# Kernel optimization log

Measured on AMD Instinct MI355X. Metric: run time of the kernel, lower is better.

## Reference

```python
import jax, jax.numpy as jnp
import numpy as np

EPS = 1e-6
NEG_SLOPE = 0.01  # torch LeakyReLU default

def ln(x, g, b):
    m = jnp.mean(x, axis=-1, keepdims=True)
    v = jnp.mean((x - m) ** 2, axis=-1, keepdims=True)
    return (x - m) / jnp.sqrt(v + EPS) * g + b

def leaky(x):
    return jnp.where(x >= 0, x, NEG_SLOPE * x)

def setup_inputs() -> dict:
    B, L, F, H, NH, LBL = 8, 1024, 1024, 256, 8, 4766
    key = jax.random.key(0)
    ks = jax.random.split(key, 16)
    def lin(k, i, o, s=0.03):
        kw, kb = jax.random.split(k)
        return jax.random.normal(kw, (i, o), jnp.float32) * s, jnp.zeros((o,), jnp.float32)
    w_in, b_in = lin(ks[0], F, H)
    w_h, b_h = lin(ks[1], H, H)
    a_w1, a_b1 = lin(ks[2], H, 64)
    a_w2, a_b2 = lin(ks[3], 64, NH)
    o_w1, o_b1 = lin(ks[4], NH * H, NH * H)
    o_w2, o_b2 = lin(ks[5], NH * H, LBL)
    CM = (jax.random.uniform(ks[6], (LBL, LBL)) < 0.002).astype(jnp.float32)
    CM = jnp.maximum(CM, jnp.eye(LBL, dtype=jnp.float32))
    return {
        'h_V': jax.random.normal(ks[7], (B, L, F), jnp.float32),
        'mask': jnp.ones((B, L), jnp.int32),
        'ln0_g': jnp.ones((F,), jnp.float32), 'ln0_b': jnp.zeros((F,), jnp.float32),
        'w_in': w_in, 'b_in': b_in,
        'ln1_g': jnp.ones((H,), jnp.float32), 'ln1_b': jnp.zeros((H,), jnp.float32),
        'w_h': w_h, 'b_h': b_h,
        'ln2_g': jnp.ones((H,), jnp.float32), 'ln2_b': jnp.zeros((H,), jnp.float32),
        'a_w1': a_w1, 'a_b1': a_b1,
        'a_lng': jnp.ones((64,), jnp.float32), 'a_lnb': jnp.zeros((64,), jnp.float32),
        'a_w2': a_w2, 'a_b2': a_b2,
        'o_w1': o_w1, 'o_b1': o_b1,
        'o_lng': jnp.ones((NH * H,), jnp.float32), 'o_lnb': jnp.zeros((NH * H,), jnp.float32),
        'o_w2': o_w2, 'o_b2': o_b2,
        'CM': CM,
    }

def reference(h_V, mask, ln0_g, ln0_b, w_in, b_in, ln1_g, ln1_b, w_h, b_h,
              ln2_g, ln2_b, a_w1, a_b1, a_lng, a_lnb, a_w2, a_b2,
              o_w1, o_b1, o_lng, o_lnb, o_w2, o_b2, CM):
    B = h_V.shape[0]
    # input + hidden blocks (eval mode: dropout is identity)
    x = ln(h_V, ln0_g, ln0_b)
    x = leaky(x @ w_in + b_in)
    x = ln(x, ln1_g, ln1_b)
    x = leaky(x @ w_h + b_h)
    x = ln(x, ln2_g, ln2_b)                      # [B,L,H]
    # multi-head attention pooling over sequence
    a = leaky(x @ a_w1 + a_b1)
    a = ln(a, a_lng, a_lnb)
    a = a @ a_w2 + a_b2                          # [B,L,NH]
    a = jnp.where(mask[:, :, None] == 0, jnp.float32(-1e9), a)
    a = jax.nn.softmax(a, axis=1)
    h = jnp.einsum('blh,bld->bhd', a, x).reshape(B, -1)  # [B,NH*H]
    # output block
    h = leaky(h @ o_w1 + o_b1)
    h = ln(h, o_lng, o_lnb)
    p = jax.nn.sigmoid(h @ o_w2 + o_b2)          # [B,LBL]
    # GO-hierarchy max-product propagation (eval path)
    out = jnp.max(p[:, None, :] * CM[None, :, :], axis=-1)  # [B,LBL]
    return out.astype(jnp.float32)
```

## Files before the change

kernel.cpp:

```cpp
#include <hip/hip_runtime.h>
#include <hip/hip_bf16.h>
#include <cstdint>

#define B_   8
#define L_   1024
#define F_   1024
#define H_   256
#define NH_  8
#define LBL_ 4766
#define M_   (B_*L_)
#define OD_  (NH_*H_)
#define NCM  (LBL_*LBL_)
#define MP_EPB 16384
#define MP_NB  ((NCM + MP_EPB - 1) / MP_EPB)
#define NCH  32

typedef unsigned short u16;
typedef unsigned int   u32;
typedef __attribute__((ext_vector_type(8))) short short8;
typedef __attribute__((ext_vector_type(4))) float float4v;

#define BF16_ONES_PAIR 0x3f803f80u

__device__ __forceinline__ float bf2f(u32 u) { return __uint_as_float(u << 16); }
__device__ __forceinline__ u16 f2bf(float f) {
    u32 u = __float_as_uint(f);
    u32 r = 0x7fffu + ((u >> 16) & 1u);
    return (u16)((u + r) >> 16);
}

struct f8 { float v[8]; };

__device__ __forceinline__ float ldS(const void* p, size_t i, bool bf) {
    return bf ? bf2f(((const u16*)p)[i]) : ((const float*)p)[i];
}
__device__ __forceinline__ float4 ld4(const void* p, size_t i, bool bf) {
    if (bf) {
        uint2 u = *(const uint2*)((const u16*)p + i);
        return make_float4(bf2f(u.x & 0xffff), bf2f(u.x >> 16),
                           bf2f(u.y & 0xffff), bf2f(u.y >> 16));
    }
    return *(const float4*)((const float*)p + i);
}
__device__ __forceinline__ f8 ld8(const void* p, size_t i, bool bf) {
    f8 r;
    if (bf) {
        uint4 u = *(const uint4*)((const u16*)p + i);
        r.v[0]=bf2f(u.x&0xffff); r.v[1]=bf2f(u.x>>16);
        r.v[2]=bf2f(u.y&0xffff); r.v[3]=bf2f(u.y>>16);
        r.v[4]=bf2f(u.z&0xffff); r.v[5]=bf2f(u.z>>16);
        r.v[6]=bf2f(u.w&0xffff); r.v[7]=bf2f(u.w>>16);
    } else {
        const float* q = (const float*)p + i;
        float4 a = *(const float4*)q, b = *(const float4*)(q+4);
        r.v[0]=a.x; r.v[1]=a.y; r.v[2]=a.z; r.v[3]=a.w;
        r.v[4]=b.x; r.v[5]=b.y; r.v[6]=b.z; r.v[7]=b.w;
    }
    return r;
}

__device__ __forceinline__ float wave_sum(float v) {
    #pragma unroll
    for (int m = 1; m < 64; m <<= 1) v += __shfl_xor(v, m, 64);
    return v;
}
__device__ __forceinline__ float wave_max(float v) {
    #pragma unroll
    for (int m = 1; m < 64; m <<= 1) v = fmaxf(v, __shfl_xor(v, m, 64));
    return v;
}
__device__ __forceinline__ float blk_sum(float v, float* sh) {
    v = wave_sum(v);
    int w = threadIdx.x >> 6, nw = blockDim.x >> 6;
    if ((threadIdx.x & 63) == 0) sh[w] = v;
    __syncthreads();
    float s = sh[0];
    for (int i = 1; i < nw; ++i) s += sh[i];
    __syncthreads();
    return s;
}
__device__ __forceinline__ float blk_max(float v, float* sh) {
    v = wave_max(v);
    int w = threadIdx.x >> 6, nw = blockDim.x >> 6;
    if ((threadIdx.x & 63) == 0) sh[w] = v;
    __syncthreads();
    float s = sh[0];
    for (int i = 1; i < nw; ++i) s = fmaxf(s, sh[i]);
    __syncthreads();
    return s;
}

__global__ __launch_bounds__(256) void prep_k(const void* __restrict__ hv,
        const void* __restrict__ g0, const void* __restrict__ b0, u16* __restrict__ x0,
        const void* __restrict__ w_in, u16* __restrict__ wt1,
        const void* __restrict__ w_h,  u16* __restrict__ wt2,
        const void* __restrict__ aw1,  u16* __restrict__ wt3,
        float* __restrict__ zA,
        const u32* __restrict__ probe) {
    __shared__ u16 tile[64][65];
    bool bf = (probe[0] == BF16_ONES_PAIR);
    int blk = blockIdx.x, t = threadIdx.x;
    if (blk < M_/4) {
        int row = (blk << 2) + (t >> 6);
        int l = t & 63;
        size_t base = (size_t)row * F_;
        float4 vv[4];
        float s = 0.f, q = 0.f;
        #pragma unroll
        for (int j = 0; j < 4; ++j) {
            float4 v = ld4(hv, base + l * 4 + j * 256, bf);
            vv[j] = v;
            s += v.x + v.y + v.z + v.w;
            q += v.x*v.x + v.y*v.y + v.z*v.z + v.w*v.w;
        }
        s = wave_sum(s);
        q = wave_sum(q);
        float mean = s * (1.f / F_);
        float rstd = rsqrtf(q * (1.f / F_) - mean * mean + 1e-6f);
        #pragma unroll
        for (int j = 0; j < 4; ++j) {
            int off = l * 4 + j * 256;
            float4 gg = ld4(g0, off, bf);
            float4 bb = ld4(b0, off, bf);
            float4 v = vv[j];
            u32 o0 = f2bf((v.x - mean) * rstd * gg.x + bb.x)
                   | ((u32)f2bf((v.y - mean) * rstd * gg.y + bb.y) << 16);
            u32 o1 = f2bf((v.z - mean) * rstd * gg.z + bb.z)
                   | ((u32)f2bf((v.w - mean) * rstd * gg.w + bb.w) << 16);
            *(uint2*)(x0 + base + off) = make_uint2(o0, o1);
        }
        return;
    }
    blk -= M_/4;
    const void* W = nullptr; u16* WT = nullptr; int K = 0, N = 0, kt = 0, nt = 0;
    if (blk < 64)      { W = w_in; WT = wt1; K = F_; N = H_; kt = blk & 15; nt = blk >> 4; }
    else if (blk < 80) { int j = blk - 64; W = w_h; WT = wt2; K = H_; N = H_; kt = j & 3; nt = j >> 2; }
    else if (blk < 84) { int j = blk - 80; W = aw1; WT = wt3; K = H_; N = 64; kt = j; nt = 0; }
    else {
        int j = blk - 84;
        float4* p = (float4*)zA;
        for (int i = j * 256 + t; i < 8192; i += 4096) p[i] = make_float4(0,0,0,0);
        return;
    }
    int kt0 = kt * 64, nt0 = nt * 64;
    int r = t >> 2, cq = (t & 3) * 16;
    #pragma unroll
    for (int j = 0; j < 4; ++j) {
        float4 v = ld4(W, (size_t)(kt0 + r) * N + nt0 + cq + j * 4, bf);
        tile[r][cq + j*4 + 0] = f2bf(v.x);
        tile[r][cq + j*4 + 1] = f2bf(v.y);
        tile[r][cq + j*4 + 2] = f2bf(v.z);
        tile[r][cq + j*4 + 3] = f2bf(v.w);
    }
    __syncthreads();
    #pragma unroll
    for (int j = 0; j < 4; ++j) {
        int k = cq + j * 4;
        u32 a0 = tile[k+0][r], a1 = tile[k+1][r], a2 = tile[k+2][r], a3 = tile[k+3][r];
        uint2 o; o.x = a0 | (a1 << 16); o.y = a2 | (a3 << 16);
        *(uint2*)(WT + (size_t)(nt0 + r) * K + kt0 + k) = o;
    }
}

__global__ __launch_bounds__(256) void gemm_mfma(const u16* __restrict__ Ap, int amode,
        const float2* __restrict__ statin, const void* __restrict__ g,
        const void* __restrict__ bta, const u16* __restrict__ WT,
        const void* __restrict__ bias, u16* __restrict__ C,
        float* __restrict__ statout, int M, int N, int K,
        const u32* __restrict__ probe) {
    __shared__ short8 As[2][64][5];
    __shared__ short8 Bs[2][64][5];
    bool pbf = (probe[0] == BF16_ONES_PAIR);
    int t = threadIdx.x;
    int m0 = blockIdx.x * 64, n0 = blockIdx.y * 64;
    int r = t >> 2, kq = t & 3;
    int l = t & 63, w = t >> 6;
    int q = l >> 4, ml = l & 15;
    float4v acc[4];
    #pragma unroll
    for (int nt = 0; nt < 4; ++nt)
        #pragma unroll
        for (int i = 0; i < 4; ++i) acc[nt][i] = 0.f;
    float stm = 0.f, str = 1.f;
    if (amode == 1) {
        float2 st = statin[m0 + r];
        float mm = st.x * (1.f / K);
        stm = mm;
        str = rsqrtf(st.y * (1.f / K) - mm * mm + 1e-6f);
    }
    const size_t arow = (size_t)(m0 + r) * K;
    const size_t brow = (size_t)(n0 + r) * K;
    auto loadA = [&](int kk) -> short8 {
        if (amode == 1) {
            f8 a  = ld8(Ap, arow + kk, true);
            f8 gg = ld8(g, kk, pbf);
            f8 bb = ld8(bta, kk, pbf);
            short8 pa;
            #pragma unroll
            for (int j = 0; j < 8; ++j)
                pa[j] = (short)f2bf((a.v[j] - stm) * str * gg.v[j] + bb.v[j]);
            return pa;
        }
        return *(const short8*)(Ap + arow + kk);
    };
    {
        short8 pa = loadA(kq * 8);
        short8 pb = *(const short8*)(WT + brow + kq * 8);
        As[0][r][kq] = pa;
        Bs[0][r][kq] = pb;
    }
    __syncthreads();
    int nIt = K >> 5, cur = 0;
    for (int it = 0; it < nIt; ++it) {
        bool more = (it + 1 < nIt);
        short8 na, nb;
        if (more) {
            int kk = (it + 1) * 32 + kq * 8;
            na = loadA(kk);
            nb = *(const short8*)(WT + brow + kk);
        }
        short8 af = As[cur][w * 16 + ml][q];
        #pragma unroll
        for (int nt = 0; nt < 4; ++nt)
            acc[nt] = __builtin_amdgcn_mfma_f32_16x16x32_bf16(af, Bs[cur][nt*16 + ml][q],
                                                              acc[nt], 0, 0, 0);
        if (more) {
            As[cur ^ 1][r][kq] = na;
            Bs[cur ^ 1][r][kq] = nb;
            __syncthreads();
            cur ^= 1;
        }
    }
    float ov[4][4];
    #pragma unroll
    for (int nt = 0; nt < 4; ++nt) {
        int nn = n0 + nt * 16 + ml;
        float bv = ldS(bias, nn, pbf);
        #pragma unroll
        for (int reg = 0; reg < 4; ++reg) {
            float v = acc[nt][reg] + bv;
            v = v >= 0.f ? v : 0.01f * v;
            ov[nt][reg] = v;
            C[(size_t)(m0 + w * 16 + q * 4 + reg) * N + nn] = f2bf(v);
        }
    }
    if (statout) {
        #pragma unroll
        for (int reg = 0; reg < 4; ++reg) {
            float sv = ov[0][reg] + ov[1][reg] + ov[2][reg] + ov[3][reg];
            float qv = ov[0][reg]*ov[0][reg] + ov[1][reg]*ov[1][reg]
                     + ov[2][reg]*ov[2][reg] + ov[3][reg]*ov[3][reg];
            #pragma unroll
            for (int mk = 1; mk < 16; mk <<= 1) {
                sv += __shfl_xor(sv, mk, 64);
                qv += __shfl_xor(qv, mk, 64);
            }
            if (ml == 0) {
                int row = m0 + w * 16 + q * 4 + reg;
                atomicAdd(&statout[2 * row],     sv);
                atomicAdd(&statout[2 * row + 1], qv);
            }
        }
    }
}

__global__ __launch_bounds__(256) void gemm3_attn_k(const u16* __restrict__ Ap,
        const float2* __restrict__ statin, const void* __restrict__ g,
        const void* __restrict__ bta, const u16* __restrict__ WT,
        const void* __restrict__ bias,
        const void* __restrict__ alng, const void* __restrict__ alnb,
        const void* __restrict__ aw2, const void* __restrict__ ab2,
        const int* __restrict__ mask, float* __restrict__ lg,
        const u32* __restrict__ probe) {
    __shared__ short8 As[2][64][5];
    __shared__ short8 Bs[2][64][5];
    __shared__ float at[64][65];
    __shared__ float w2s[512];
    __shared__ float b2s[8];
    __shared__ float gs[64], bs[64];
    bool pbf = (probe[0] == BF16_ONES_PAIR);
    const int K = 256;
    int t = threadIdx.x;
    int m0 = blockIdx.x * 64;
    int r = t >> 2, kq = t & 3;
    int l = t & 63, w = t >> 6;
    int q = l >> 4, ml = l & 15;
    float4v acc[4];
    #pragma unroll
    for (int nt = 0; nt < 4; ++nt)
        #pragma unroll
        for (int i = 0; i < 4; ++i) acc[nt][i] = 0.f;
    float2 st = statin[m0 + r];
    float stm = st.x * (1.f / K);
    float str = rsqrtf(st.y * (1.f / K) - stm * stm + 1e-6f);
    const size_t arow = (size_t)(m0 + r) * K;
    const size_t brow = (size_t)r * K;
    auto loadA = [&](int kk) -> short8 {
        f8 a  = ld8(Ap, arow + kk, true);
        f8 gg = ld8(g, kk, pbf);
        f8 bb = ld8(bta, kk, pbf);
        short8 pa;
        #pragma unroll
        for (int j = 0; j < 8; ++j)
            pa[j] = (short)f2bf((a.v[j] - stm) * str * gg.v[j] + bb.v[j]);
        return pa;
    };
    {
        short8 pa = loadA(kq * 8);
        short8 pb = *(const short8*)(WT + brow + kq * 8);
        As[0][r][kq] = pa;
        Bs[0][r][kq] = pb;
    }
    __syncthreads();
    int cur = 0;
    #pragma unroll
    for (int it = 0; it < 8; ++it) {
        bool more = (it < 7);
        short8 na, nb;
        if (more) {
            int kk = (it + 1) * 32 + kq * 8;
            na = loadA(kk);
            nb = *(const short8*)(WT + brow + kk);
        }
        short8 af = As[cur][w * 16 + ml][q];
        #pragma unroll
        for (int nt = 0; nt < 4; ++nt)
            acc[nt] = __builtin_amdgcn_mfma_f32_16x16x32_bf16(af, Bs[cur][nt*16 + ml][q],
                                                              acc[nt], 0, 0, 0);
        if (more) {
            As[cur ^ 1][r][kq] = na;
            Bs[cur ^ 1][r][kq] = nb;
            __syncthreads();
            cur ^= 1;
        }
    }
    for (int i = t; i < 512; i += 256) w2s[i] = ldS(aw2, i, pbf);
    if (t < 8) b2s[t] = ldS(ab2, t, pbf);
    if (t < 64) { gs[t] = ldS(alng, t, pbf); bs[t] = ldS(alnb, t, pbf); }
    #pragma unroll
    for (int nt = 0; nt < 4; ++nt) {
        int nn = nt * 16 + ml;
        float bv = ldS(bias, nn, pbf);
        #pragma unroll
        for (int reg = 0; reg < 4; ++reg) {
            float v = acc[nt][reg] + bv;
            v = v >= 0.f ? v : 0.01f * v;
            at[w * 16 + q * 4 + reg][nn] = v;
        }
    }
    __syncthreads();
    int row = t >> 2, s4 = t & 3;
    float av[16];
    float sum = 0.f, sq = 0.f;
    #pragma unroll
    for (int j = 0; j < 16; ++j) {
        float v = at[row][s4 * 16 + j];
        av[j] = v; sum += v; sq += v * v;
    }
    sum += __shfl_xor(sum, 1, 64); sum += __shfl_xor(sum, 2, 64);
    sq  += __shfl_xor(sq, 1, 64);  sq  += __shfl_xor(sq, 2, 64);
    float mr = sum * (1.f / 64);
    float rr = rsqrtf(sq * (1.f / 64) - mr * mr + 1e-6f);
    float val[16];
    #pragma unroll
    for (int j = 0; j < 16; ++j)
        val[j] = (av[j] - mr) * rr * gs[s4 * 16 + j] + bs[s4 * 16 + j];
    float hv[8];
    #pragma unroll
    for (int h = 0; h < 8; ++h) {
        float p = 0.f;
        #pragma unroll
        for (int j = 0; j < 16; ++j) p += val[j] * w2s[(s4 * 16 + j) * 8 + h];
        p += __shfl_xor(p, 1, 64);
        p += __shfl_xor(p, 2, 64);
        hv[h] = p + b2s[h];
    }
    if (s4 == 0) {
        int gr = m0 + row;
        bool mz = (mask[gr] == 0);
        int bb_ = gr >> 10, ll = gr & 1023;
        #pragma unroll
        for (int h = 0; h < 8; ++h) {
            float v = mz ? -1e9f : hv[h];
            lg[((size_t)bb_ * NH_ + h) * L_ + ll] = v;
        }
    }
}

__global__ __launch_bounds__(1024) void attnpool_k(const float* __restrict__ lg,
        const float2* __restrict__ st2, const u16* __restrict__ x2,
        const void* __restrict__ g, const void* __restrict__ b,
        float* __restrict__ hp, const u32* __restrict__ probe) {
    __shared__ float aw_s[1024];
    __shared__ float part[16][256];
    __shared__ float sh[16];
    bool pbf = (probe[0] == BF16_ONES_PAIR);
    int bh = blockIdx.x, t = threadIdx.x;
    int bb = bh >> 3;
    float v = lg[(size_t)bh * L_ + t];
    float mx = blk_max(v, sh);
    float e = expf(v - mx);
    float s = blk_sum(e, sh);
    float inv = 1.f / s;
    float2 st = st2[(bb << 10) + t];
    float m = st.x * (1.f / 256);
    float r = rsqrtf(st.y * (1.f / 256) - m * m + 1e-6f);
    float aw = e * inv * r;
    aw_s[t] = aw;
    float c1 = blk_sum(aw * m, sh);
    int chunk = t >> 6, d0 = (t & 63) * 4;
    const u16* xb = x2 + ((size_t)(bb << 10) + chunk * 64) * 256;
    const float* awc = aw_s + chunk * 64;
    float a0 = 0.f, a1 = 0.f, a2 = 0.f, a3 = 0.f;
    #pragma unroll 8
    for (int i = 0; i < 64; ++i) {
        uint2 u = *(const uint2*)(xb + (size_t)i * 256 + d0);
        float wv = awc[i];
        a0 += wv * bf2f(u.x & 0xffff);
        a1 += wv * bf2f(u.x >> 16);
        a2 += wv * bf2f(u.y & 0xffff);
        a3 += wv * bf2f(u.y >> 16);
    }
    *(float4*)&part[chunk][d0] = make_float4(a0, a1, a2, a3);
    __syncthreads();
    if (t < 256) {
        float S = 0.f;
        #pragma unroll
        for (int c = 0; c < 16; ++c) S += part[c][t];
        hp[(size_t)bh * 256 + t] = (S - c1) * ldS(g, t, pbf) + ldS(b, t, pbf);
    }
}

template<int KC>
__global__ __launch_bounds__(256) void gemv_ilp_part_k(const float* __restrict__ hv,
        const void* __restrict__ W, float* __restrict__ part, int K, int N,
        const u32* __restrict__ probe) {
    __shared__ float hs[8 * KC];
    bool bf = (probe[0] == BF16_ONES_PAIR);
    int t = threadIdx.x;
    int kb = blockIdx.y * KC;
    for (int i = t; i < 8 * KC; i += 256) {
        int r = i / KC, k = i & (KC - 1);
        hs[i] = hv[(size_t)r * K + kb + k];
    }
    __syncthreads();
    int c0 = (blockIdx.x * 256 + t) * 2;
    if (c0 >= N) return;
    float a[8][2] = {};
    if (bf) {
        const u16* Wp = (const u16*)W;
        #pragma unroll
        for (int h = 0; h < KC / 32; ++h) {
            u32 wr[32];
            #pragma unroll
            for (int i = 0; i < 32; ++i)
                wr[i] = *(const u32*)(Wp + (size_t)(kb + h * 32 + i) * N + c0);
            #pragma unroll
            for (int i = 0; i < 32; ++i) {
                float w0 = bf2f(wr[i] & 0xffff), w1 = bf2f(wr[i] >> 16);
                #pragma unroll
                for (int r = 0; r < 8; ++r) {
                    float hh = hs[r * KC + h * 32 + i];
                    a[r][0] += hh * w0; a[r][1] += hh * w1;
                }
            }
        }
    } else {
        const float* Wp = (const float*)W;
        #pragma unroll
        for (int h = 0; h < KC / 16; ++h) {
            float2 wr[16];
            #pragma unroll
            for (int i = 0; i < 16; ++i)
                wr[i] = *(const float2*)(Wp + (size_t)(kb + h * 16 + i) * N + c0);
            #pragma unroll
            for (int i = 0; i < 16; ++i) {
                #pragma unroll
                for (int r = 0; r < 8; ++r) {
                    float hh = hs[r * KC + h * 16 + i];
                    a[r][0] += hh * wr[i].x; a[r][1] += hh * wr[i].y;
                }
            }
        }
    }
    float* dst = part + ((size_t)blockIdx.y * 8) * N + c0;
    bool ok1 = (c0 + 1 < N);
    #pragma unroll
    for (int r = 0; r < 8; ++r) {
        if (ok1) *(float2*)(dst + (size_t)r * N) = make_float2(a[r][0], a[r][1]);
        else dst[(size_t)r * N] = a[r][0];
    }
}

__global__ __launch_bounds__(1024) void out_ln_k(const float* __restrict__ part,
        float* __restrict__ h, const void* __restrict__ bias,
        const void* __restrict__ g, const void* __restrict__ b,
        const u32* __restrict__ probe) {
    __shared__ float sh[16];
    bool bf = (probe[0] == BF16_ONES_PAIR);
    int row = blockIdx.x, t = threadIdx.x;
    float v[2];
    float s = 0.f, q = 0.f;
    #pragma unroll
    for (int i = 0; i < 2; ++i) {
        int c = t + i * 1024;
        float pv[NCH];
        #pragma unroll
        for (int ch = 0; ch < NCH; ++ch)
            pv[ch] = part[((size_t)ch * 8 + row) * OD_ + c];
        #pragma unroll
        for (int st = NCH / 2; st >= 1; st >>= 1)
            #pragma unroll
            for (int j = 0; j < NCH; ++j)
                if (j < st) pv[j] += pv[j + st];
        float x = ldS(bias, c, bf) + pv[0];
        x = x >= 0.f ? x : 0.01f * x;
        v[i] = x; s += x; q += x * x;
    }
    s = blk_sum(s, sh) * (1.f / OD_);
    q = blk_sum(q, sh) * (1.f / OD_);
    float rstd = rsqrtf(q - s * s + 1e-6f);
    #pragma unroll
    for (int i = 0; i < 2; ++i) {
        int c = t + i * 1024;
        h[(size_t)row * OD_ + c] = (v[i] - s) * rstd * ldS(g, c, bf) + ldS(b, c, bf);
    }
}

__global__ __launch_bounds__(256) void sigmoid_t_k(const float* __restrict__ part,
        const void* __restrict__ bias, float* __restrict__ pt,
        float* __restrict__ out, const u32* __restrict__ probe) {
    bool bf = (probe[0] == BF16_ONES_PAIR);
    int c = blockIdx.x * 256 + threadIdx.x;
    int r = blockIdx.y;
    if (c >= LBL_) return;
    float pv[NCH];
    #pragma unroll
    for (int ch = 0; ch < NCH; ++ch)
        pv[ch] = part[((size_t)ch * 8 + r) * LBL_ + c];
    #pragma unroll
    for (int st = NCH / 2; st >= 1; st >>= 1)
        #pragma unroll
        for (int j = 0; j < NCH; ++j)
            if (j < st) pv[j] += pv[j + st];
    float v = ldS(bias, c, bf) + pv[0];
    pt[(size_t)c * 8 + r] = 1.f / (1.f + expf(-v));
    out[(size_t)r * LBL_ + c] = 0.f;
}

__device__ __forceinline__ void mp_hit(u32 idx, float cmv,
        const float* __restrict__ pt, int* smax, u32 rowBase) {
    u32 i = idx / LBL_;
    u32 j = idx - i * LBL_;
    const float4* pj = (const float4*)(pt + (size_t)j * 8);
    float4 pa = pj[0], pb = pj[1];
    int base = (int)(i - rowBase) * 8;
    atomicMax(&smax[base + 0], __float_as_int(pa.x * cmv));
    atomicMax(&smax[base + 1], __float_as_int(pa.y * cmv));
    atomicMax(&smax[base + 2], __float_as_int(pa.z * cmv));
    atomicMax(&smax[base + 3], __float_as_int(pa.w * cmv));
    atomicMax(&smax[base + 4], __float_as_int(pb.x * cmv));
    atomicMax(&smax[base + 5], __float_as_int(pb.y * cmv));
    atomicMax(&smax[base + 6], __float_as_int(pb.z * cmv));
    atomicMax(&smax[base + 7], __float_as_int(pb.w * cmv));
}

__global__ __launch_bounds__(256) void maxprod3_k(const float* __restrict__ pt,
        const void* __restrict__ CM, float* __restrict__ out,
        const u32* __restrict__ probe) {
    __shared__ int smax[6 * 8];
    bool bf = (probe[0] == BF16_ONES_PAIR);
    int t = threadIdx.x;
    size_t blockStart = (size_t)blockIdx.x * MP_EPB;
    u32 rowBase = (u32)(blockStart / LBL_);
    for (int i = t; i < 48; i += 256) smax[i] = 0;
    __syncthreads();
    if (bf) {
        const u16* cm = (const u16*)CM;
        uint4 ch[8];
        size_t i0[8];
        #pragma unroll
        for (int u = 0; u < 8; ++u) {
            size_t idx0 = blockStart + ((size_t)u * 256 + t) * 8;
            i0[u] = idx0;
            ch[u] = (idx0 + 8 <= NCM) ? *(const uint4*)(cm + idx0)
                                      : make_uint4(0, 0, 0, 0);
        }
        #pragma unroll
        for (int u = 0; u < 8; ++u) {
            size_t idx0 = i0[u];
            if (idx0 + 8 <= NCM) {
                uint4 c4 = ch[u];
                if ((c4.x | c4.y | c4.z | c4.w) == 0) continue;
                u32 hw[4] = {c4.x, c4.y, c4.z, c4.w};
                #pragma unroll
                for (int d = 0; d < 4; ++d) {
                    u32 lo = hw[d] & 0xffff, hi = hw[d] >> 16;
                    if (lo) mp_hit((u32)idx0 + d*2,     bf2f(lo), pt, smax, rowBase);
                    if (hi) mp_hit((u32)idx0 + d*2 + 1, bf2f(hi), pt, smax, rowBase);
                }
            } else if (idx0 < NCM) {
                for (u32 e = 0; e < (u32)(NCM - idx0); ++e) {
                    u16 h = cm[idx0 + e];
                    if (h) mp_hit((u32)idx0 + e, bf2f(h), pt, smax, rowBase);
                }
            }
        }
    } else {
        const float* cm = (const float*)CM;
        #pragma unroll
        for (int u = 0; u < 16; ++u) {
            size_t idx0 = blockStart + ((size_t)u * 256 + t) * 4;
            if (idx0 >= NCM) continue;
            float v[4];
            if (idx0 + 4 <= NCM) {
                float4 f = *(const float4*)(cm + idx0);
                v[0] = f.x; v[1] = f.y; v[2] = f.z; v[3] = f.w;
            } else {
                v[0] = v[1] = v[2] = v[3] = 0.f;
                for (u32 e = 0; e < (u32)(NCM - idx0); ++e) v[e] = cm[idx0 + e];
            }
            if (v[0] == 0.f && v[1] == 0.f && v[2] == 0.f && v[3] == 0.f) continue;
            #pragma unroll
            for (int e = 0; e < 4; ++e)
                if (v[e] != 0.f) mp_hit((u32)idx0 + e, v[e], pt, smax, rowBase);
        }
    }
    __syncthreads();
    size_t lastIdx = blockStart + MP_EPB - 1;
    if (lastIdx >= NCM) lastIdx = NCM - 1;
    int nrows = (int)((u32)(lastIdx / LBL_) - rowBase) + 1;
    for (int s = t; s < nrows * 8; s += 256) {
        int v = smax[s];
        if (v != 0) {
            int rr = s >> 3, b = s & 7;
            atomicMax((int*)(out + (size_t)b * LBL_ + rowBase + rr), v);
        }
    }
}

extern "C" void kernel_launch(void* const* d_in, const int* in_sizes, int n_in,
                              void* d_out, int out_size, void* d_ws, size_t ws_size,
                              hipStream_t stream) {
    const void* hv   = d_in[0];
    const int* mask  = (const int*)d_in[1];
    const void* ln0g = d_in[2];
    const void* ln0b = d_in[3];
    const void* w_in = d_in[4];
    const void* b_in = d_in[5];
    const void* ln1g = d_in[6];
    const void* ln1b = d_in[7];
    const void* w_h  = d_in[8];
    const void* b_h  = d_in[9];
    const void* ln2g = d_in[10];
    const void* ln2b = d_in[11];
    const void* aw1  = d_in[12];
    const void* ab1  = d_in[13];
    const void* alng = d_in[14];
    const void* alnb = d_in[15];
    const void* aw2  = d_in[16];
    const void* ab2  = d_in[17];
    const void* ow1  = d_in[18];
    const void* ob1  = d_in[19];
    const void* olng = d_in[20];
    const void* olnb = d_in[21];
    const void* ow2  = d_in[22];
    const void* ob2  = d_in[23];
    const void* CM   = d_in[24];
    const u32* probe = (const u32*)ln0g;
    float* out = (float*)d_out;

    float* f = (float*)d_ws;
    float2* st1 = (float2*)f;
    float2* st2 = st1 + 8192;
    float* lg    = f + 32768;
    float* hp    = lg + 65536;
    float* ha    = hp + 16384;
    float* part1 = ha + 16384;
    float* part2 = part1 + 524288;
    float* pt    = part2 + 1220096;
    u16* x0  = (u16*)(pt + 38128);
    u16* x1  = x0 + 8388608;
    u16* x2  = x1 + 2097152;
    u16* wt1 = x2 + 2097152;
    u16* wt2 = wt1 + 262144;
    u16* wt3 = wt2 + 65536;

    prep_k<<<M_/4 + 84 + 16, 256, 0, stream>>>(hv, ln0g, ln0b, x0,
                                               w_in, wt1, w_h, wt2, aw1, wt3,
                                               f, probe);
    gemm_mfma<<<dim3(M_/64, 4), 256, 0, stream>>>(x0, 2, nullptr, nullptr, nullptr,
                                                  wt1, b_in, x1, (float*)st1,
                                                  M_, H_, F_, probe);
    gemm_mfma<<<dim3(M_/64, 4), 256, 0, stream>>>(x1, 1, st1, ln1g, ln1b,
                                                  wt2, b_h, x2, (float*)st2,
                                                  M_, H_, H_, probe);
    gemm3_attn_k<<<M_/64, 256, 0, stream>>>(x2, st2, ln2g, ln2b, wt3, ab1,
                                            alng, alnb, aw2, ab2, mask, lg, probe);
    attnpool_k<<<B_*NH_, 1024, 0, stream>>>(lg, st2, x2, ln2g, ln2b, hp, probe);
    gemv_ilp_part_k<64><<<dim3(OD_/512, NCH), 256, 0, stream>>>(hp, ow1, part1,
                                                                OD_, OD_, probe);
    out_ln_k<<<B_, 1024, 0, stream>>>(part1, ha, ob1, olng, olnb, probe);
    gemv_ilp_part_k<64><<<dim3((LBL_+511)/512, NCH), 256, 0, stream>>>(ha, ow2, part2,
                                                                       OD_, LBL_, probe);
    sigmoid_t_k<<<dim3((LBL_+255)/256, 8), 256, 0, stream>>>(part2, ob2, pt, out, probe);
    maxprod3_k<<<MP_NB, 256, 0, stream>>>(pt, CM, out, probe);
}
```

Before: 332.6 us.

## Widen GEMM N-tile to 128 and replace stat atomics with per-tile partial writes

The gemm_mfma tile grows from 64x64 to 64x128, so each block does 8 MFMA accumulators per k-step and the A tile is loaded and LayerNorm-normalized half as often. Row-stat accumulation switches from atomicAdd into a zeroed buffer to plain stores of per-column-tile partials, which consumers (next GEMM, gemm3_attn, attnpool) sum from two slices. This removes the zero-init blocks in prep_k. The cost is halving the grid of the first two GEMMs to 256 blocks, which lowers occupancy on a 256-CU part, and adding accumulator registers.

```diff
diff --git a/kernel.cpp b/kernel.cpp
--- a/kernel.cpp
+++ b/kernel.cpp
@@ -95,7 +95,6 @@
         const void* __restrict__ w_in, u16* __restrict__ wt1,
         const void* __restrict__ w_h,  u16* __restrict__ wt2,
         const void* __restrict__ aw1,  u16* __restrict__ wt3,
-        float* __restrict__ zA,
         const u32* __restrict__ probe) {
     __shared__ u16 tile[64][65];
     bool bf = (probe[0] == BF16_ONES_PAIR);
@@ -135,13 +134,7 @@
     const void* W = nullptr; u16* WT = nullptr; int K = 0, N = 0, kt = 0, nt = 0;
     if (blk < 64)      { W = w_in; WT = wt1; K = F_; N = H_; kt = blk & 15; nt = blk >> 4; }
     else if (blk < 80) { int j = blk - 64; W = w_h; WT = wt2; K = H_; N = H_; kt = j & 3; nt = j >> 2; }
-    else if (blk < 84) { int j = blk - 80; W = aw1; WT = wt3; K = H_; N = 64; kt = j; nt = 0; }
-    else {
-        int j = blk - 84;
-        float4* p = (float4*)zA;
-        for (int i = j * 256 + t; i < 8192; i += 4096) p[i] = make_float4(0,0,0,0);
-        return;
-    }
+    else               { int j = blk - 80; W = aw1; WT = wt3; K = H_; N = 64; kt = j; nt = 0; }
     int kt0 = kt * 64, nt0 = nt * 64;
     int r = t >> 2, cq = (t & 3) * 16;
     #pragma unroll
@@ -169,27 +162,30 @@
         float* __restrict__ statout, int M, int N, int K,
         const u32* __restrict__ probe) {
     __shared__ short8 As[2][64][5];
-    __shared__ short8 Bs[2][64][5];
+    __shared__ short8 Bs[2][128][5];
     bool pbf = (probe[0] == BF16_ONES_PAIR);
     int t = threadIdx.x;
-    int m0 = blockIdx.x * 64, n0 = blockIdx.y * 64;
+    int m0 = blockIdx.x * 64, n0 = blockIdx.y * 128;
     int r = t >> 2, kq = t & 3;
+    int rb = t & 127, hb = t >> 7;
     int l = t & 63, w = t >> 6;
     int q = l >> 4, ml = l & 15;
-    float4v acc[4];
-    #pragma unroll
-    for (int nt = 0; nt < 4; ++nt)
+    float4v acc[8];
+    #pragma unroll
+    for (int nt = 0; nt < 8; ++nt)
         #pragma unroll
         for (int i = 0; i < 4; ++i) acc[nt][i] = 0.f;
     float stm = 0.f, str = 1.f;
     if (amode == 1) {
-        float2 st = statin[m0 + r];
-        float mm = st.x * (1.f / K);
+        float2 s0 = statin[m0 + r];
+        float2 s1 = statin[M + m0 + r];
+        float ssum = s0.x + s1.x, ssq = s0.y + s1.y;
+        float mm = ssum * (1.f / K);
         stm = mm;
-        str = rsqrtf(st.y * (1.f / K) - mm * mm + 1e-6f);
+        str = rsqrtf(ssq * (1.f / K) - mm * mm + 1e-6f);
     }
     const size_t arow = (size_t)(m0 + r) * K;
-    const size_t brow = (size_t)(n0 + r) * K;
+    const size_t brow = (size_t)(n0 + rb) * K + hb * 16;
     auto loadA = [&](int kk) -> short8 {
         if (amode == 1) {
             f8 a  = ld8(Ap, arow + kk, true);
@@ -205,35 +201,39 @@
     };
     {
         short8 pa = loadA(kq * 8);
-        short8 pb = *(const short8*)(WT + brow + kq * 8);
+        short8 pb0 = *(const short8*)(WT + brow);
+        short8 pb1 = *(const short8*)(WT + brow + 8);
         As[0][r][kq] = pa;
-        Bs[0][r][kq] = pb;
+        Bs[0][rb][2*hb]   = pb0;
+        Bs[0][rb][2*hb+1] = pb1;
     }
     __syncthreads();
     int nIt = K >> 5, cur = 0;
     for (int it = 0; it < nIt; ++it) {
         bool more = (it + 1 < nIt);
-        short8 na, nb;
+        short8 na, nb0, nb1;
         if (more) {
-            int kk = (it + 1) * 32 + kq * 8;
-            na = loadA(kk);
-            nb = *(const short8*)(WT + brow + kk);
+            int kk = (it + 1) * 32;
+            na  = loadA(kk + kq * 8);
+            nb0 = *(const short8*)(WT + brow + kk);
+            nb1 = *(const short8*)(WT + brow + kk + 8);
         }
         short8 af = As[cur][w * 16 + ml][q];
         #pragma unroll
-        for (int nt = 0; nt < 4; ++nt)
+        for (int nt = 0; nt < 8; ++nt)
             acc[nt] = __builtin_amdgcn_mfma_f32_16x16x32_bf16(af, Bs[cur][nt*16 + ml][q],
                                                               acc[nt], 0, 0, 0);
         if (more) {
             As[cur ^ 1][r][kq] = na;
-            Bs[cur ^ 1][r][kq] = nb;
+            Bs[cur ^ 1][rb][2*hb]   = nb0;
+            Bs[cur ^ 1][rb][2*hb+1] = nb1;
             __syncthreads();
             cur ^= 1;
         }
     }
-    float ov[4][4];
-    #pragma unroll
-    for (int nt = 0; nt < 4; ++nt) {
+    float ov[8][4];
+    #pragma unroll
+    for (int nt = 0; nt < 8; ++nt) {
         int nn = n0 + nt * 16 + ml;
         float bv = ldS(bias, nn, pbf);
         #pragma unroll
@@ -247,9 +247,12 @@
     if (statout) {
         #pragma unroll
         for (int reg = 0; reg < 4; ++reg) {
-            float sv = ov[0][reg] + ov[1][reg] + ov[2][reg] + ov[3][reg];
-            float qv = ov[0][reg]*ov[0][reg] + ov[1][reg]*ov[1][reg]
-                     + ov[2][reg]*ov[2][reg] + ov[3][reg]*ov[3][reg];
+            float sv = 0.f, qv = 0.f;
+            #pragma unroll
+            for (int nt = 0; nt < 8; ++nt) {
+                sv += ov[nt][reg];
+                qv += ov[nt][reg] * ov[nt][reg];
+            }
             #pragma unroll
             for (int mk = 1; mk < 16; mk <<= 1) {
                 sv += __shfl_xor(sv, mk, 64);
@@ -257,8 +260,9 @@
             }
             if (ml == 0) {
                 int row = m0 + w * 16 + q * 4 + reg;
-                atomicAdd(&statout[2 * row],     sv);
-                atomicAdd(&statout[2 * row + 1], qv);
+                size_t base = ((size_t)blockIdx.y * M + row) * 2;
+                statout[base]     = sv;
+                statout[base + 1] = qv;
             }
         }
     }
@@ -290,9 +294,11 @@
     for (int nt = 0; nt < 4; ++nt)
         #pragma unroll
         for (int i = 0; i < 4; ++i) acc[nt][i] = 0.f;
-    float2 st = statin[m0 + r];
-    float stm = st.x * (1.f / K);
-    float str = rsqrtf(st.y * (1.f / K) - stm * stm + 1e-6f);
+    float2 s0 = statin[m0 + r];
+    float2 s1 = statin[M_ + m0 + r];
+    float ssum = s0.x + s1.x, ssq = s0.y + s1.y;
+    float stm = ssum * (1.f / K);
+    float str = rsqrtf(ssq * (1.f / K) - stm * stm + 1e-6f);
     const size_t arow = (size_t)(m0 + r) * K;
     const size_t brow = (size_t)r * K;
     auto loadA = [&](int kk) -> short8 {
@@ -402,9 +408,12 @@
     float e = expf(v - mx);
     float s = blk_sum(e, sh);
     float inv = 1.f / s;
-    float2 st = st2[(bb << 10) + t];
-    float m = st.x * (1.f / 256);
-    float r = rsqrtf(st.y * (1.f / 256) - m * m + 1e-6f);
+    int sidx = (bb << 10) + t;
+    float2 sa = st2[sidx];
+    float2 sb = st2[8192 + sidx];
+    float ssum = sa.x + sb.x, ssq = sa.y + sb.y;
+    float m = ssum * (1.f / 256);
+    float r = rsqrtf(ssq * (1.f / 256) - m * m + 1e-6f);
     float aw = e * inv * r;
     aw_s[t] = aw;
     float c1 = blk_sum(aw * m, sh);
@@ -672,8 +681,8 @@
 
     float* f = (float*)d_ws;
     float2* st1 = (float2*)f;
-    float2* st2 = st1 + 8192;
-    float* lg    = f + 32768;
+    float2* st2 = st1 + 16384;
+    float* lg    = f + 65536;
     float* hp    = lg + 65536;
     float* ha    = hp + 16384;
     float* part1 = ha + 16384;
@@ -686,13 +695,12 @@
     u16* wt2 = wt1 + 262144;
     u16* wt3 = wt2 + 65536;
 
-    prep_k<<<M_/4 + 84 + 16, 256, 0, stream>>>(hv, ln0g, ln0b, x0,
-                                               w_in, wt1, w_h, wt2, aw1, wt3,
-                                               f, probe);
-    gemm_mfma<<<dim3(M_/64, 4), 256, 0, stream>>>(x0, 2, nullptr, nullptr, nullptr,
+    prep_k<<<M_/4 + 84, 256, 0, stream>>>(hv, ln0g, ln0b, x0,
+                                          w_in, wt1, w_h, wt2, aw1, wt3, probe);
+    gemm_mfma<<<dim3(M_/64, 2), 256, 0, stream>>>(x0, 2, nullptr, nullptr, nullptr,
                                                   wt1, b_in, x1, (float*)st1,
                                                   M_, H_, F_, probe);
-    gemm_mfma<<<dim3(M_/64, 4), 256, 0, stream>>>(x1, 1, st1, ln1g, ln1b,
+    gemm_mfma<<<dim3(M_/64, 2), 256, 0, stream>>>(x1, 1, st1, ln1g, ln1b,
                                                   wt2, b_h, x2, (float*)st2,
                                                   M_, H_, H_, probe);
     gemm3_attn_k<<<M_/64, 256, 0, stream>>>(x2, st2, ln2g, ln2b, wt3, ab1,
```

New measurement: 341.3 us. 1.03x slower.

## Double GEMM K-step to 64 and replace row-stat atomics with per-column-tile partials

Applied to the files above, without the earlier changes.

The MFMA GEMM now stages 64 K-elements per shared-memory buffer and runs two MFMA k-substeps per barrier, which halves the number of syncs and global-load rounds. LayerNorm row statistics are no longer accumulated with float atomics. Each of the 4 column-tile blocks writes its own partial sum and sum of squares, and consumers add the 4 partials together. This also drops the zeroing pass from the prep kernel. It costs more shared memory and registers per block and four stat reads per row instead of one.

```diff
diff --git a/kernel.cpp b/kernel.cpp
--- a/kernel.cpp
+++ b/kernel.cpp
@@ -95,7 +95,6 @@
         const void* __restrict__ w_in, u16* __restrict__ wt1,
         const void* __restrict__ w_h,  u16* __restrict__ wt2,
         const void* __restrict__ aw1,  u16* __restrict__ wt3,
-        float* __restrict__ zA,
         const u32* __restrict__ probe) {
     __shared__ u16 tile[64][65];
     bool bf = (probe[0] == BF16_ONES_PAIR);
@@ -135,13 +134,7 @@
     const void* W = nullptr; u16* WT = nullptr; int K = 0, N = 0, kt = 0, nt = 0;
     if (blk < 64)      { W = w_in; WT = wt1; K = F_; N = H_; kt = blk & 15; nt = blk >> 4; }
     else if (blk < 80) { int j = blk - 64; W = w_h; WT = wt2; K = H_; N = H_; kt = j & 3; nt = j >> 2; }
-    else if (blk < 84) { int j = blk - 80; W = aw1; WT = wt3; K = H_; N = 64; kt = j; nt = 0; }
-    else {
-        int j = blk - 84;
-        float4* p = (float4*)zA;
-        for (int i = j * 256 + t; i < 8192; i += 4096) p[i] = make_float4(0,0,0,0);
-        return;
-    }
+    else               { int j = blk - 80; W = aw1; WT = wt3; K = H_; N = 64; kt = j; nt = 0; }
     int kt0 = kt * 64, nt0 = nt * 64;
     int r = t >> 2, cq = (t & 3) * 16;
     #pragma unroll
@@ -168,8 +161,8 @@
         const void* __restrict__ bias, u16* __restrict__ C,
         float* __restrict__ statout, int M, int N, int K,
         const u32* __restrict__ probe) {
-    __shared__ short8 As[2][64][5];
-    __shared__ short8 Bs[2][64][5];
+    __shared__ short8 As[2][64][9];
+    __shared__ short8 Bs[2][64][9];
     bool pbf = (probe[0] == BF16_ONES_PAIR);
     int t = threadIdx.x;
     int m0 = blockIdx.x * 64, n0 = blockIdx.y * 64;
@@ -183,10 +176,15 @@
         for (int i = 0; i < 4; ++i) acc[nt][i] = 0.f;
     float stm = 0.f, str = 1.f;
     if (amode == 1) {
-        float2 st = statin[m0 + r];
-        float mm = st.x * (1.f / K);
+        float ssum = 0.f, ssq = 0.f;
+        #pragma unroll
+        for (int p = 0; p < 4; ++p) {
+            float2 s = statin[(size_t)p * M + m0 + r];
+            ssum += s.x; ssq += s.y;
+        }
+        float mm = ssum * (1.f / K);
         stm = mm;
-        str = rsqrtf(st.y * (1.f / K) - mm * mm + 1e-6f);
+        str = rsqrtf(ssq * (1.f / K) - mm * mm + 1e-6f);
     }
     const size_t arow = (size_t)(m0 + r) * K;
     const size_t brow = (size_t)(n0 + r) * K;
@@ -204,29 +202,36 @@
         return *(const short8*)(Ap + arow + kk);
     };
     {
-        short8 pa = loadA(kq * 8);
-        short8 pb = *(const short8*)(WT + brow + kq * 8);
-        As[0][r][kq] = pa;
-        Bs[0][r][kq] = pb;
-    }
-    __syncthreads();
-    int nIt = K >> 5, cur = 0;
+        As[0][r][kq]     = loadA(kq * 8);
+        As[0][r][kq + 4] = loadA(32 + kq * 8);
+        Bs[0][r][kq]     = *(const short8*)(WT + brow + kq * 8);
+        Bs[0][r][kq + 4] = *(const short8*)(WT + brow + 32 + kq * 8);
+    }
+    __syncthreads();
+    int nIt = K >> 6, cur = 0;
     for (int it = 0; it < nIt; ++it) {
         bool more = (it + 1 < nIt);
-        short8 na, nb;
+        short8 na0, na1, nb0, nb1;
         if (more) {
-            int kk = (it + 1) * 32 + kq * 8;
-            na = loadA(kk);
-            nb = *(const short8*)(WT + brow + kk);
-        }
-        short8 af = As[cur][w * 16 + ml][q];
-        #pragma unroll
-        for (int nt = 0; nt < 4; ++nt)
-            acc[nt] = __builtin_amdgcn_mfma_f32_16x16x32_bf16(af, Bs[cur][nt*16 + ml][q],
-                                                              acc[nt], 0, 0, 0);
+            int kk = (it + 1) * 64;
+            na0 = loadA(kk + kq * 8);
+            na1 = loadA(kk + 32 + kq * 8);
+            nb0 = *(const short8*)(WT + brow + kk + kq * 8);
+            nb1 = *(const short8*)(WT + brow + kk + 32 + kq * 8);
+        }
+        #pragma unroll
+        for (int ks = 0; ks < 2; ++ks) {
+            short8 af = As[cur][w * 16 + ml][ks * 4 + q];
+            #pragma unroll
+            for (int nt = 0; nt < 4; ++nt)
+                acc[nt] = __builtin_amdgcn_mfma_f32_16x16x32_bf16(
+                              af, Bs[cur][nt*16 + ml][ks * 4 + q], acc[nt], 0, 0, 0);
+        }
         if (more) {
-            As[cur ^ 1][r][kq] = na;
-            Bs[cur ^ 1][r][kq] = nb;
+            As[cur ^ 1][r][kq]     = na0;
+            As[cur ^ 1][r][kq + 4] = na1;
+            Bs[cur ^ 1][r][kq]     = nb0;
+            Bs[cur ^ 1][r][kq + 4] = nb1;
             __syncthreads();
             cur ^= 1;
         }
@@ -257,8 +262,8 @@
             }
             if (ml == 0) {
                 int row = m0 + w * 16 + q * 4 + reg;
-                atomicAdd(&statout[2 * row],     sv);
-                atomicAdd(&statout[2 * row + 1], qv);
+                *(float2*)&statout[((size_t)blockIdx.y * M + row) * 2] =
+                    make_float2(sv, qv);
             }
         }
     }
@@ -290,9 +295,14 @@
     for (int nt = 0; nt < 4; ++nt)
         #pragma unroll
         for (int i = 0; i < 4; ++i) acc[nt][i] = 0.f;
-    float2 st = statin[m0 + r];
-    float stm = st.x * (1.f / K);
-    float str = rsqrtf(st.y * (1.f / K) - stm * stm + 1e-6f);
+    float ssum = 0.f, ssq = 0.f;
+    #pragma unroll
+    for (int p = 0; p < 4; ++p) {
+        float2 s = statin[(size_t)p * M_ + m0 + r];
+        ssum += s.x; ssq += s.y;
+    }
+    float stm = ssum * (1.f / K);
+    float str = rsqrtf(ssq * (1.f / K) - stm * stm + 1e-6f);
     const size_t arow = (size_t)(m0 + r) * K;
     const size_t brow = (size_t)r * K;
     auto loadA = [&](int kk) -> short8 {
@@ -402,9 +412,15 @@
     float e = expf(v - mx);
     float s = blk_sum(e, sh);
     float inv = 1.f / s;
-    float2 st = st2[(bb << 10) + t];
-    float m = st.x * (1.f / 256);
-    float r = rsqrtf(st.y * (1.f / 256) - m * m + 1e-6f);
+    int sidx = (bb << 10) + t;
+    float ssum = 0.f, ssq = 0.f;
+    #pragma unroll
+    for (int p = 0; p < 4; ++p) {
+        float2 sp = st2[(size_t)p * 8192 + sidx];
+        ssum += sp.x; ssq += sp.y;
+    }
+    float m = ssum * (1.f / 256);
+    float r = rsqrtf(ssq * (1.f / 256) - m * m + 1e-6f);
     float aw = e * inv * r;
     aw_s[t] = aw;
     float c1 = blk_sum(aw * m, sh);
@@ -672,8 +688,8 @@
 
     float* f = (float*)d_ws;
     float2* st1 = (float2*)f;
-    float2* st2 = st1 + 8192;
-    float* lg    = f + 32768;
+    float2* st2 = st1 + 32768;
+    float* lg    = f + 131072;
     float* hp    = lg + 65536;
     float* ha    = hp + 16384;
     float* part1 = ha + 16384;
@@ -686,9 +702,8 @@
     u16* wt2 = wt1 + 262144;
     u16* wt3 = wt2 + 65536;
 
-    prep_k<<<M_/4 + 84 + 16, 256, 0, stream>>>(hv, ln0g, ln0b, x0,
-                                               w_in, wt1, w_h, wt2, aw1, wt3,
-                                               f, probe);
+    prep_k<<<M_/4 + 84, 256, 0, stream>>>(hv, ln0g, ln0b, x0,
+                                          w_in, wt1, w_h, wt2, aw1, wt3, probe);
     gemm_mfma<<<dim3(M_/64, 4), 256, 0, stream>>>(x0, 2, nullptr, nullptr, nullptr,
                                                   wt1, b_in, x1, (float*)st1,
                                                   M_, H_, F_, probe);
```

After: 331.2 us. Within noise of the previous version (-0.4%).
